# Performance work log

Measured on AMD Instinct MI355X. Metric: run time of the kernel, lower is better.

Reference implementation:

```python
import jax, jax.numpy as jnp
import numpy as np

EPS = 1e-5

def _layer_norm(y, w, b):
    mu = y.mean(-1, keepdims=True)
    var = jnp.mean((y - mu) ** 2, axis=-1, keepdims=True)
    return (y - mu) * jax.lax.rsqrt(var + EPS) * w + b


def setup_inputs() -> dict:
    key = jax.random.key(0)
    ks = jax.random.split(key, 8)
    B, D, H, W = 1, 96, 96, 96
    N, R, K = 16, 6, 4
    x = jax.random.normal(ks[0], (B, D, H, W), jnp.float32)
    x_proj_weight = jax.random.normal(ks[1], (K, R + 2 * N, D), jnp.float32) * 0.05
    dt_projs_weight = jax.random.normal(ks[2], (K, D, R), jnp.float32) * 0.1
    dt_projs_bias = jax.random.normal(ks[3], (K, D), jnp.float32) * 0.1
    A_logs = jax.random.normal(ks[4], (K * D, N), jnp.float32)
    Ds = jax.random.normal(ks[5], (K * D,), jnp.float32) * 0.1
    ln_w = jnp.ones((D,), jnp.float32)
    ln_b = jnp.zeros((D,), jnp.float32)
    return {"x": x, "x_proj_weight": x_proj_weight, "dt_projs_weight": dt_projs_weight,
            "dt_projs_bias": dt_projs_bias, "A_logs": A_logs, "Ds": Ds,
            "ln_w": ln_w, "ln_b": ln_b}


def reference(x, x_proj_weight, dt_projs_weight, dt_projs_bias, A_logs, Ds, ln_w, ln_b):
    B, D, H, W = x.shape
    L = H * W
    K = x_proj_weight.shape[0]            # 4 scan directions
    N = A_logs.shape[1]                   # d_state
    R = dt_projs_weight.shape[2]          # dt_rank

    # ---- CrossScan: 4 directional flattenings -> xs [B, K, D, L]
    xs0 = x.reshape(B, D, L)
    xs1 = jnp.swapaxes(x, 2, 3).reshape(B, D, L)
    xs = jnp.stack([xs0, xs1, xs0[:, :, ::-1], xs1[:, :, ::-1]], axis=1)

    # ---- input-dependent projections
    x_dbl = jnp.einsum('bkdl,kcd->bkcl', xs, x_proj_weight)    # [B,K,R+2N,L]
    dts = x_dbl[:, :, :R]
    Bs = x_dbl[:, :, R:R + N]                                  # [B,K,N,L]
    Cs = x_dbl[:, :, R + N:]                                   # [B,K,N,L]
    dts = jnp.einsum('bkrl,kdr->bkdl', dts, dt_projs_weight)   # [B,K,D,L]

    # ---- selective scan (S6), delta_softplus=True, fp32
    delta = jax.nn.softplus(dts + dt_projs_bias[None, :, :, None])   # [B,K,D,L]
    A = -jnp.exp(A_logs).reshape(K, D, N)                             # [K,D,N]
    dA = jnp.exp(jnp.einsum('bkdl,kdn->bkdln', delta, A))             # [B,K,D,L,N]
    dBu = jnp.einsum('bkdl,bknl,bkdl->bkdln', delta, Bs, xs)          # delta*B*u

    def combine(c1, c2):
        a1, b1 = c1
        a2, b2 = c2
        return a1 * a2, a2 * b1 + b2

    _, h = jax.lax.associative_scan(combine, (dA, dBu), axis=3)       # h_t over L

    y = jnp.einsum('bkdln,bknl->bkdl', h, Cs)
    y = y + xs * Ds.reshape(K, D)[None, :, :, None]                   # [B,K,D,L]

    # ---- CrossMerge: undo the 4 directional scans and sum
    ys = y[:, 0:2] + y[:, 2:4, :, ::-1]                               # [B,2,D,L]
    ym = ys[:, 0] + jnp.swapaxes(ys[:, 1].reshape(B, D, W, H), 2, 3).reshape(B, D, L)

    # ---- out_norm (LayerNorm over D) and reshape to [B,H,W,D]
    yout = jnp.swapaxes(ym, 1, 2)                                     # [B,L,D]
    yout = _layer_norm(yout, ln_w, ln_b).reshape(B, H, W, D)
    return yout.astype(x.dtype)
```

## Files before the change

kernel.cpp:

```cpp
#include <hip/hip_runtime.h>
#include <math.h>

constexpr int cD = 96, cL = 9216, cK = 4;
constexpr int CL = 72, NCH = 128;
constexpr long cDL = (long)cD * cL;
constexpr float LOG2E = 1.44269504088896f;

constexpr long OFF_XT    = 0;
constexpr long OFF_DELTA = OFF_XT    + cDL;
constexpr long OFF_BS    = OFF_DELTA + 4L*cDL;
constexpr long OFF_CS    = OFF_BS    + 4L*cL*16;
constexpr long OFF_Y     = OFF_CS    + 4L*cL*16;
constexpr long OFF_YT    = OFF_Y     + 4L*cDL;

__device__ __forceinline__ float4 a2prep(float4 v) {
    return make_float4(-LOG2E * exp2f(LOG2E * v.x), -LOG2E * exp2f(LOG2E * v.y),
                       -LOG2E * exp2f(LOG2E * v.z), -LOG2E * exp2f(LOG2E * v.w));
}
template<int C>
__device__ __forceinline__ float qperm(float v) {
    return __int_as_float(__builtin_amdgcn_mov_dpp(__float_as_int(v), C, 0xf, 0xf, true));
}

__global__ __launch_bounds__(256) void kT(const float* __restrict__ x,
                                          float* __restrict__ xT) {
    __shared__ float t[32][33];
    const int h0 = blockIdx.x * 32, w0 = blockIdx.y * 32, d = blockIdx.z;
    const float* xd = x + (long)d * cL;
    float* xtd = xT + (long)d * cL;
    for (int o = threadIdx.x; o < 1024; o += 256) {
        int i = o >> 5, j = o & 31;
        t[i][j] = xd[(h0 + i) * 96 + w0 + j];
    }
    __syncthreads();
    for (int o = threadIdx.x; o < 1024; o += 256) {
        int i = o >> 5, j = o & 31;
        xtd[(w0 + i) * 96 + h0 + j] = t[j][i];
    }
}

__global__ __launch_bounds__(256) void kA(const float* __restrict__ x,
                                          const float* __restrict__ xT,
                                          const float* __restrict__ xpw,
                                          const float* __restrict__ dtw,
                                          const float* __restrict__ dtb,
                                          float* __restrict__ delta,
                                          float* __restrict__ Bs,
                                          float* __restrict__ Cs) {
    __shared__ float xs[96][64];
    __shared__ float xdbl[38][65];
    __shared__ float dtw_l[96 * 6];
    __shared__ float dtb_l[96];
    const int p0 = blockIdx.x * 64;
    const int k  = blockIdx.y;
    const int tid = threadIdx.x;
    const float* src = (k & 1) ? xT : x;

    for (int o = tid; o < 96 * 64; o += 256) {
        int dd = o >> 6, pp = o & 63;
        xs[dd][pp] = src[(long)dd * cL + p0 + pp];
    }
    for (int o = tid; o < 96 * 6; o += 256) dtw_l[o] = dtw[k * 96 * 6 + o];
    if (tid < 96) dtb_l[tid] = dtb[k * 96 + tid];
    __syncthreads();

    const int lane = tid & 63;
    const int c0 = __builtin_amdgcn_readfirstlane((tid >> 6) * 10);
    const float* wk = xpw + (long)k * 38 * 96;
    float acc[10];
    #pragma unroll
    for (int i = 0; i < 10; ++i) acc[i] = 0.f;
    #pragma unroll 4
    for (int dd = 0; dd < 96; ++dd) {
        float xv = xs[dd][lane];
        #pragma unroll
        for (int i = 0; i < 10; ++i) {
            int c = c0 + i; c = c > 37 ? 37 : c;
            acc[i] = fmaf(xv, wk[c * 96 + dd], acc[i]);
        }
    }
    #pragma unroll
    for (int i = 0; i < 10; ++i) {
        int c = c0 + i; c = c > 37 ? 37 : c;
        xdbl[c][lane] = acc[i];
    }
    __syncthreads();

    for (int o = tid; o < 64 * 16; o += 256) {
        int n = o & 15, pp = o >> 4;
        int P = p0 + pp;
        int q = (k < 2) ? P : (9215 - P);
        int ch = q / 72, j = q - ch * 72;
        long idx = (((long)k * 72 + j) * 128 + ch) * 16 + n;
        Bs[idx] = xdbl[6 + n][pp];
        Cs[idx] = xdbl[22 + n][pp];
    }
    for (int o = tid; o < 96 * 64; o += 256) {
        int dd = o >> 6, pp = o & 63;
        float s = dtb_l[dd];
        #pragma unroll
        for (int r = 0; r < 6; ++r) s = fmaf(xdbl[r][pp], dtw_l[dd * 6 + r], s);
        float sp = fmaxf(s, 0.f) + __logf(1.f + __expf(-fabsf(s)));
        delta[((long)(k * 96 + dd)) * cL + p0 + pp] = sp;
    }
}

__global__ __launch_bounds__(512, 2) void kS(const float* __restrict__ x,
                                             const float* __restrict__ xT,
                                             const float* __restrict__ delta,
                                             const float* __restrict__ Bs,
                                             const float* __restrict__ Cs,
                                             const float* __restrict__ Alog,
                                             const float* __restrict__ Dsv,
                                             float* __restrict__ y) {
    __shared__ float lp[NCH][16];
    __shared__ float ls[NCH][16];
    float* gpf = &lp[0][0];
    const int tid = threadIdx.x;
    const int seq = blockIdx.x;
    const int k = seq / 96, d = seq % 96, rev = k >> 1;
    const int n0 = (tid & 3) * 4, ch = tid >> 2;
    const int r = tid & 3;
    const int q0 = rev ? (9215 - ch * CL) : ch * CL;

    const float4 a2 = a2prep(*(const float4*)(Alog + (long)seq * 16 + n0));
    const float Dv = Dsv[seq];
    const float* dB = delta + (long)seq * cL + q0;
    const float* xB = ((k & 1) ? xT : x) + (long)d * cL + q0;
    const float* bB = Bs + (long)k * cL * 16 + (long)ch * 16 + n0;
    const float* cB = Cs + (long)k * cL * 16 + (long)ch * 16 + n0;

    float4 h = make_float4(0.f, 0.f, 0.f, 0.f);
    float sdl = 0.f;
#define S1(DL, XV, OFF) { \
        float4 B = *(const float4*)(bB + (OFF) * 2048); \
        float t = (DL) * (XV); sdl += (DL); \
        h.x = fmaf(exp2f((DL)*a2.x), h.x, t*B.x); \
        h.y = fmaf(exp2f((DL)*a2.y), h.y, t*B.y); \
        h.z = fmaf(exp2f((DL)*a2.z), h.z, t*B.z); \
        h.w = fmaf(exp2f((DL)*a2.w), h.w, t*B.w); }
    if (!rev) {
        #pragma unroll
        for (int g = 0; g < 18; ++g) {
            float4 d4 = *(const float4*)(dB + 4*g);
            float4 x4 = *(const float4*)(xB + 4*g);
            S1(d4.x, x4.x, 4*g)   S1(d4.y, x4.y, 4*g+1)
            S1(d4.z, x4.z, 4*g+2) S1(d4.w, x4.w, 4*g+3)
        }
    } else {
        #pragma unroll
        for (int g = 0; g < 18; ++g) {
            float4 d4 = *(const float4*)(dB - 4*g - 3);
            float4 x4 = *(const float4*)(xB - 4*g - 3);
            S1(d4.w, x4.w, 4*g)   S1(d4.z, x4.z, 4*g+1)
            S1(d4.y, x4.y, 4*g+2) S1(d4.x, x4.x, 4*g+3)
        }
    }
#undef S1
    *(float4*)&lp[ch][n0] = make_float4(exp2f(a2.x*sdl), exp2f(a2.y*sdl),
                                        exp2f(a2.z*sdl), exp2f(a2.w*sdl));
    *(float4*)&ls[ch][n0] = h;
    __syncthreads();

    const int sn = tid & 15, sg = tid >> 4;
    float LPe[4], LSe[4];
    {
        float P = 1.f, S = 0.f;
        #pragma unroll
        for (int i = 0; i < 4; ++i) {
            LPe[i] = P; LSe[i] = S;
            float p = lp[sg * 4 + i][sn], s = ls[sg * 4 + i][sn];
            S = fmaf(p, S, s); P = p * P;
        }
        __syncthreads();
        gpf[tid] = P; gpf[512 + tid] = S;
    }
    __syncthreads();
    #pragma unroll
    for (int off = 1; off < 32; off <<= 1) {
        float pc = gpf[tid], sc = gpf[512 + tid];
        float pn = pc, snn = sc;
        if (sg >= off) {
            pn  = pc * gpf[tid - off * 16];
            snn = fmaf(pc, gpf[512 + tid - off * 16], sc);
        }
        __syncthreads();
        gpf[tid] = pn; gpf[512 + tid] = snn;
        __syncthreads();
    }
    const float GS = (sg == 0) ? 0.f : gpf[512 + tid - 16];
    #pragma unroll
    for (int i = 0; i < 4; ++i) ls[sg * 4 + i][sn] = fmaf(LPe[i], GS, LSe[i]);
    __syncthreads();

    h = *(float4*)&ls[ch][n0];
    float* yq = y + (long)seq * cL + ch * CL;
    float yhold = 0.f;
#define S2(DL, XV, SI, OFF) { \
        float4 B = *(const float4*)(bB + (OFF) * 2048); \
        float4 C = *(const float4*)(cB + (OFF) * 2048); \
        float t = (DL) * (XV); \
        h.x = fmaf(exp2f((DL)*a2.x), h.x, t*B.x); \
        h.y = fmaf(exp2f((DL)*a2.y), h.y, t*B.y); \
        h.z = fmaf(exp2f((DL)*a2.z), h.z, t*B.z); \
        h.w = fmaf(exp2f((DL)*a2.w), h.w, t*B.w); \
        float pv = fmaf(h.x, C.x, fmaf(h.y, C.y, fmaf(h.z, C.z, h.w * C.w))); \
        pv += qperm<0xB1>(pv); \
        pv += qperm<0x4E>(pv); \
        if ((SI) == r) yhold = fmaf(Dv, (XV), pv); }
    if (!rev) {
        #pragma unroll
        for (int g = 0; g < 18; ++g) {
            float4 d4 = *(const float4*)(dB + 4*g);
            float4 x4 = *(const float4*)(xB + 4*g);
            S2(d4.x, x4.x, 0, 4*g)   S2(d4.y, x4.y, 1, 4*g+1)
            S2(d4.z, x4.z, 2, 4*g+2) S2(d4.w, x4.w, 3, 4*g+3)
            yq[4*g + r] = yhold;
        }
    } else {
        #pragma unroll
        for (int g = 0; g < 18; ++g) {
            float4 d4 = *(const float4*)(dB - 4*g - 3);
            float4 x4 = *(const float4*)(xB - 4*g - 3);
            S2(d4.w, x4.w, 0, 4*g)   S2(d4.z, x4.z, 1, 4*g+1)
            S2(d4.y, x4.y, 2, 4*g+2) S2(d4.x, x4.x, 3, 4*g+3)
            yq[4*g + r] = yhold;
        }
    }
#undef S2
}

__global__ __launch_bounds__(256) void kU(const float* __restrict__ Y,
                                          float* __restrict__ YT) {
    __shared__ float t[32][33];
    const int i0 = blockIdx.x * 32, j0 = blockIdx.y * 32;
    const int z = blockIdx.z;
    const int arr = z / 96, d = z % 96;
    const float* src = Y + (1 + 2 * arr) * cDL + (long)d * cL;
    float* dst = YT + (long)arr * cDL + (long)d * cL;
    for (int o = threadIdx.x; o < 1024; o += 256) {
        int i = o >> 5, j = o & 31;
        t[i][j] = src[(i0 + i) * 96 + j0 + j];
    }
    __syncthreads();
    for (int o = threadIdx.x; o < 1024; o += 256) {
        int i = o >> 5, j = o & 31;
        dst[(j0 + i) * 96 + i0 + j] = t[j][i];
    }
}

__global__ __launch_bounds__(256) void kE(const float* __restrict__ Y,
                                          const float* __restrict__ YT,
                                          const float* __restrict__ lnw,
                                          const float* __restrict__ lnb,
                                          float* __restrict__ out) {
    __shared__ float vs[96][36];
    __shared__ float red[8][32], red2[8][32];
    __shared__ float MU[32], RS[32];
    const int tid = threadIdx.x;
    const int p0 = blockIdx.x * 32;

    for (int o = tid; o < 96 * 8; o += 256) {
        int dd = o >> 3, j = o & 7;
        const float* r0 = Y + (long)dd * cL + p0;
        const float* r1 = YT + (long)dd * cL + p0;
        const float* r2 = Y + 2 * cDL + (long)dd * cL;
        const float* r3 = YT + cDL + (long)dd * cL;
        float4 a = ((const float4*)r0)[j];
        float4 b = ((const float4*)r1)[j];
        float4 c = *(const float4*)(r2 + 9212 - p0 - 4 * j);
        float4 e = *(const float4*)(r3 + 9212 - p0 - 4 * j);
        *(float4*)&vs[dd][4 * j] = make_float4(a.x + b.x + c.w + e.w,
                                               a.y + b.y + c.z + e.z,
                                               a.z + b.z + c.y + e.y,
                                               a.w + b.w + c.x + e.x);
    }
    __syncthreads();

    const int p = tid & 31, part = tid >> 5;
    float s = 0.f, s2 = 0.f;
    for (int dd = part * 12; dd < part * 12 + 12; ++dd) {
        float v = vs[dd][p];
        s += v; s2 = fmaf(v, v, s2);
    }
    red[part][p] = s; red2[part][p] = s2;
    __syncthreads();
    if (tid < 32) {
        float S = 0.f, S2 = 0.f;
        #pragma unroll
        for (int q = 0; q < 8; ++q) { S += red[q][tid]; S2 += red2[q][tid]; }
        float m = S * (1.f / 96.f);
        MU[tid] = m;
        RS[tid] = rsqrtf(S2 * (1.f / 96.f) - m * m + 1e-5f);
    }
    __syncthreads();
    for (int o = tid; o < 32 * 96; o += 256) {
        int pl = o / 96, dd = o - pl * 96;
        out[(long)(p0 + pl) * 96 + dd] = (vs[dd][pl] - MU[pl]) * RS[pl] * lnw[dd] + lnb[dd];
    }
}

extern "C" void kernel_launch(void* const* d_in, const int* in_sizes, int n_in,
                              void* d_out, int out_size, void* d_ws, size_t ws_size,
                              hipStream_t stream) {
    const float* x    = (const float*)d_in[0];
    const float* xpw  = (const float*)d_in[1];
    const float* dtw  = (const float*)d_in[2];
    const float* dtb  = (const float*)d_in[3];
    const float* Alog = (const float*)d_in[4];
    const float* Dsv  = (const float*)d_in[5];
    const float* lnw  = (const float*)d_in[6];
    const float* lnb  = (const float*)d_in[7];
    float* ws = (float*)d_ws;

    float* xT    = ws + OFF_XT;
    float* delta = ws + OFF_DELTA;
    float* Bs    = ws + OFF_BS;
    float* Cs    = ws + OFF_CS;
    float* y     = ws + OFF_Y;
    float* yT    = ws + OFF_YT;
    float* out   = (float*)d_out;

    kT<<<dim3(3, 3, 96), 256, 0, stream>>>(x, xT);
    kA<<<dim3(144, 4), 256, 0, stream>>>(x, xT, xpw, dtw, dtb, delta, Bs, Cs);
    kS<<<cK * cD, 512, 0, stream>>>(x, xT, delta, Bs, Cs, Alog, Dsv, y);
    kU<<<dim3(3, 3, 192), 256, 0, stream>>>(y, yT);
    kE<<<288, 256, 0, stream>>>(y, yT, lnw, lnb, out);
}
```

Measured before the change: 100.6 us.

## Halve scan chunk length, double threads per sequence, interleave B and C

The selective-scan kernel now splits each sequence into 256 chunks of 36 steps instead of 128 chunks of 72, running 1024 threads per block. This shortens the serial per-thread recurrence and adds one more step to the block-level prefix scan. B and C projections are also interleaved into a single buffer so each timestep's B and C values sit next to each other in memory. In exchange the cross-chunk combine gets longer, and 1024-thread blocks may limit registers and occupancy.

```diff
diff --git a/kernel.cpp b/kernel.cpp
--- a/kernel.cpp
+++ b/kernel.cpp
@@ -2,15 +2,14 @@
 #include <math.h>
 
 constexpr int cD = 96, cL = 9216, cK = 4;
-constexpr int CL = 72, NCH = 128;
+constexpr int CL = 36, NCH = 256;
 constexpr long cDL = (long)cD * cL;
 constexpr float LOG2E = 1.44269504088896f;
 
 constexpr long OFF_XT    = 0;
 constexpr long OFF_DELTA = OFF_XT    + cDL;
-constexpr long OFF_BS    = OFF_DELTA + 4L*cDL;
-constexpr long OFF_CS    = OFF_BS    + 4L*cL*16;
-constexpr long OFF_Y     = OFF_CS    + 4L*cL*16;
+constexpr long OFF_BC    = OFF_DELTA + 4L*cDL;
+constexpr long OFF_Y     = OFF_BC    + 4L*cL*32;
 constexpr long OFF_YT    = OFF_Y     + 4L*cDL;
 
 __device__ __forceinline__ float4 a2prep(float4 v) {
@@ -45,8 +44,7 @@
                                           const float* __restrict__ dtw,
                                           const float* __restrict__ dtb,
                                           float* __restrict__ delta,
-                                          float* __restrict__ Bs,
-                                          float* __restrict__ Cs) {
+                                          float* __restrict__ BC) {
     __shared__ float xs[96][64];
     __shared__ float xdbl[38][65];
     __shared__ float dtw_l[96 * 6];
@@ -90,10 +88,10 @@
         int n = o & 15, pp = o >> 4;
         int P = p0 + pp;
         int q = (k < 2) ? P : (9215 - P);
-        int ch = q / 72, j = q - ch * 72;
-        long idx = (((long)k * 72 + j) * 128 + ch) * 16 + n;
-        Bs[idx] = xdbl[6 + n][pp];
-        Cs[idx] = xdbl[22 + n][pp];
+        int ch = q / 36, j = q - ch * 36;
+        long idx = (((long)k * 36 + j) * 256 + ch) * 32 + n;
+        BC[idx]      = xdbl[6 + n][pp];
+        BC[idx + 16] = xdbl[22 + n][pp];
     }
     for (int o = tid; o < 96 * 64; o += 256) {
         int dd = o >> 6, pp = o & 63;
@@ -105,14 +103,13 @@
     }
 }
 
-__global__ __launch_bounds__(512, 2) void kS(const float* __restrict__ x,
-                                             const float* __restrict__ xT,
-                                             const float* __restrict__ delta,
-                                             const float* __restrict__ Bs,
-                                             const float* __restrict__ Cs,
-                                             const float* __restrict__ Alog,
-                                             const float* __restrict__ Dsv,
-                                             float* __restrict__ y) {
+__global__ __launch_bounds__(1024, 2) void kS(const float* __restrict__ x,
+                                              const float* __restrict__ xT,
+                                              const float* __restrict__ delta,
+                                              const float* __restrict__ BC,
+                                              const float* __restrict__ Alog,
+                                              const float* __restrict__ Dsv,
+                                              float* __restrict__ y) {
     __shared__ float lp[NCH][16];
     __shared__ float ls[NCH][16];
     float* gpf = &lp[0][0];
@@ -127,13 +124,12 @@
     const float Dv = Dsv[seq];
     const float* dB = delta + (long)seq * cL + q0;
     const float* xB = ((k & 1) ? xT : x) + (long)d * cL + q0;
-    const float* bB = Bs + (long)k * cL * 16 + (long)ch * 16 + n0;
-    const float* cB = Cs + (long)k * cL * 16 + (long)ch * 16 + n0;
+    const float* bcB = BC + (long)k * cL * 32 + (long)ch * 32 + n0;
 
     float4 h = make_float4(0.f, 0.f, 0.f, 0.f);
     float sdl = 0.f;
 #define S1(DL, XV, OFF) { \
-        float4 B = *(const float4*)(bB + (OFF) * 2048); \
+        float4 B = *(const float4*)(bcB + (OFF) * 8192); \
         float t = (DL) * (XV); sdl += (DL); \
         h.x = fmaf(exp2f((DL)*a2.x), h.x, t*B.x); \
         h.y = fmaf(exp2f((DL)*a2.y), h.y, t*B.y); \
@@ -141,7 +137,7 @@
         h.w = fmaf(exp2f((DL)*a2.w), h.w, t*B.w); }
     if (!rev) {
         #pragma unroll
-        for (int g = 0; g < 18; ++g) {
+        for (int g = 0; g < 9; ++g) {
             float4 d4 = *(const float4*)(dB + 4*g);
             float4 x4 = *(const float4*)(xB + 4*g);
             S1(d4.x, x4.x, 4*g)   S1(d4.y, x4.y, 4*g+1)
@@ -149,7 +145,7 @@
         }
     } else {
         #pragma unroll
-        for (int g = 0; g < 18; ++g) {
+        for (int g = 0; g < 9; ++g) {
             float4 d4 = *(const float4*)(dB - 4*g - 3);
             float4 x4 = *(const float4*)(xB - 4*g - 3);
             S1(d4.w, x4.w, 4*g)   S1(d4.z, x4.z, 4*g+1)
@@ -173,22 +169,22 @@
             S = fmaf(p, S, s); P = p * P;
         }
         __syncthreads();
-        gpf[tid] = P; gpf[512 + tid] = S;
+        gpf[tid] = P; gpf[1024 + tid] = S;
     }
     __syncthreads();
     #pragma unroll
-    for (int off = 1; off < 32; off <<= 1) {
-        float pc = gpf[tid], sc = gpf[512 + tid];
+    for (int off = 1; off < 64; off <<= 1) {
+        float pc = gpf[tid], sc = gpf[1024 + tid];
         float pn = pc, snn = sc;
         if (sg >= off) {
             pn  = pc * gpf[tid - off * 16];
-            snn = fmaf(pc, gpf[512 + tid - off * 16], sc);
+            snn = fmaf(pc, gpf[1024 + tid - off * 16], sc);
         }
         __syncthreads();
-        gpf[tid] = pn; gpf[512 + tid] = snn;
+        gpf[tid] = pn; gpf[1024 + tid] = snn;
         __syncthreads();
     }
-    const float GS = (sg == 0) ? 0.f : gpf[512 + tid - 16];
+    const float GS = (sg == 0) ? 0.f : gpf[1024 + tid - 16];
     #pragma unroll
     for (int i = 0; i < 4; ++i) ls[sg * 4 + i][sn] = fmaf(LPe[i], GS, LSe[i]);
     __syncthreads();
@@ -197,8 +193,8 @@
     float* yq = y + (long)seq * cL + ch * CL;
     float yhold = 0.f;
 #define S2(DL, XV, SI, OFF) { \
-        float4 B = *(const float4*)(bB + (OFF) * 2048); \
-        float4 C = *(const float4*)(cB + (OFF) * 2048); \
+        float4 B = *(const float4*)(bcB + (OFF) * 8192); \
+        float4 C = *(const float4*)(bcB + (OFF) * 8192 + 16); \
         float t = (DL) * (XV); \
         h.x = fmaf(exp2f((DL)*a2.x), h.x, t*B.x); \
         h.y = fmaf(exp2f((DL)*a2.y), h.y, t*B.y); \
@@ -210,7 +206,7 @@
         if ((SI) == r) yhold = fmaf(Dv, (XV), pv); }
     if (!rev) {
         #pragma unroll
-        for (int g = 0; g < 18; ++g) {
+        for (int g = 0; g < 9; ++g) {
             float4 d4 = *(const float4*)(dB + 4*g);
             float4 x4 = *(const float4*)(xB + 4*g);
             S2(d4.x, x4.x, 0, 4*g)   S2(d4.y, x4.y, 1, 4*g+1)
@@ -219,7 +215,7 @@
         }
     } else {
         #pragma unroll
-        for (int g = 0; g < 18; ++g) {
+        for (int g = 0; g < 9; ++g) {
             float4 d4 = *(const float4*)(dB - 4*g - 3);
             float4 x4 = *(const float4*)(xB - 4*g - 3);
             S2(d4.w, x4.w, 0, 4*g)   S2(d4.z, x4.z, 1, 4*g+1)
@@ -315,15 +311,14 @@
 
     float* xT    = ws + OFF_XT;
     float* delta = ws + OFF_DELTA;
-    float* Bs    = ws + OFF_BS;
-    float* Cs    = ws + OFF_CS;
+    float* BC    = ws + OFF_BC;
     float* y     = ws + OFF_Y;
     float* yT    = ws + OFF_YT;
     float* out   = (float*)d_out;
 
     kT<<<dim3(3, 3, 96), 256, 0, stream>>>(x, xT);
-    kA<<<dim3(144, 4), 256, 0, stream>>>(x, xT, xpw, dtw, dtb, delta, Bs, Cs);
-    kS<<<cK * cD, 512, 0, stream>>>(x, xT, delta, Bs, Cs, Alog, Dsv, y);
+    kA<<<dim3(144, 4), 256, 0, stream>>>(x, xT, xpw, dtw, dtb, delta, BC);
+    kS<<<cK * cD, 1024, 0, stream>>>(x, xT, delta, BC, Alog, Dsv, y);
     kU<<<dim3(3, 3, 192), 256, 0, stream>>>(y, yT);
     kE<<<288, 256, 0, stream>>>(y, yT, lnw, lnb, out);
 }
```

New measurement: 113.6 us. +12.9%, slower.
